# Performance work log

Measured on AMD Instinct MI355X. Metric: run time of the kernel, lower is better.

Reference implementation:

```python
import jax, jax.numpy as jnp
import numpy as np

VOCAB = 32
UTT_LEN = 16
NUM_MEANING_TYPES = 5
MEANINGS_PER_TYPE = 10
SUPPORT_SIZE = 100000  # = MEANINGS_PER_TYPE ** NUM_MEANING_TYPES
BATCH = 2048


def setup_inputs() -> dict:
    key = jax.random.key(0)
    k1, k2, k3 = jax.random.split(key, 3)
    # query utterances: [utt_len, batch] token ids
    utts = jax.random.randint(k1, (UTT_LEN, BATCH), 0, VOCAB, dtype=jnp.int64)
    # support set is stored as one-hot encoded utterances [S, utt_len*vocab]
    support_tokens = jax.random.randint(k2, (SUPPORT_SIZE, UTT_LEN), 0, VOCAB)
    support = jax.nn.one_hot(support_tokens, VOCAB, dtype=jnp.float32)
    support = support.reshape(SUPPORT_SIZE, UTT_LEN * VOCAB)
    # meanings table [S, num_meaning_types]
    meanings_t = jax.random.randint(k3, (SUPPORT_SIZE, NUM_MEANING_TYPES), 0,
                                    MEANINGS_PER_TYPE, dtype=jnp.int64)
    return {"utts": utts, "support": support, "meanings_t": meanings_t}


def reference(utts, support, meanings_t):
    # utts: [M, N] ints; support: [S, M*V] floats; meanings_t: [S, T] ints
    M, N = utts.shape
    # one-hot encode queries: [N, M, V] -> [N, M*V]
    batch_fluffy = jax.nn.one_hot(utts.T, VOCAB, dtype=jnp.float32).reshape(N, M * VOCAB)
    batch_sq = jnp.sum(batch_fluffy * batch_fluffy, axis=1)        # [N]
    support_sq = jnp.sum(support * support, axis=1)                # [S]
    cross = batch_fluffy @ support.T                                # [N, S]
    squared_dist = batch_sq[:, None] + support_sq[None, :] - 2.0 * cross
    # top-1 smallest distance (K=1)
    top1 = jnp.argmin(squared_dist, axis=1)                         # [N]
    meanings = meanings_t[top1]                                     # [N, T]
    return jax.nn.one_hot(meanings, MEANINGS_PER_TYPE, dtype=jnp.float32)
```

## Files before the change

### kernel.cpp

```cpp
#include <hip/hip_runtime.h>
#include <stdint.h>

#define S_ROWS 100000
#define NQ     2048
#define M_POS  16
#define VOCABS 32
#define WPB    8
#define GROUPS 8
#define CHUNKS 125
#define RC     800
#define KITER  25
#define KPAD   264

__global__ __launch_bounds__(256) void knn_decode(const float* __restrict__ support,
                                                  uint8_t* __restrict__ tok) {
    int wave = (blockIdx.x * 256 + threadIdx.x) >> 6;
    int lane = threadIdx.x & 63;
    if (wave >= S_ROWS) return;
    const float4* rowp = (const float4*)(support + (size_t)wave * 512) + lane * 2;
    float4 f0 = rowp[0];
    float4 f1 = rowp[1];
    float base = (float)((lane & 3) * 64);
    float v = f0.x * (base + 0.f)  + f0.y * (base + 8.f)  + f0.z * (base + 16.f) + f0.w * (base + 24.f)
            + f1.x * (base + 32.f) + f1.y * (base + 40.f) + f1.z * (base + 48.f) + f1.w * (base + 56.f);
    v += __shfl_xor(v, 1);
    v += __shfl_xor(v, 2);
    if ((lane & 3) == 0) {
        int p = lane >> 2;
        tok[(size_t)wave * 16 + p] = (uint8_t)(v + 0.5f);
    }
}

__device__ __forceinline__ void FA(uint32_t a, uint32_t b, uint32_t c,
                                   uint32_t& s, uint32_t& co) {
    uint32_t x = a ^ b;
    s  = x ^ c;
    co = (a & b) | (x & c);
}
__device__ __forceinline__ void HA(uint32_t a, uint32_t b, uint32_t& s, uint32_t& co) {
    s = a ^ b; co = a & b;
}

__global__ __launch_bounds__(256, 4) void knn_score(const int* __restrict__ utts,
                                                    const uint8_t* __restrict__ tok,
                                                    uint32_t* __restrict__ partial) {
    __shared__ uint32_t smem[32 * KPAD];
    uint32_t* table = smem;
    uint32_t* keys  = smem;

    const int bid = blockIdx.x;
    const int g   = bid & 7;
    const int c   = bid >> 3;
    const int t   = threadIdx.x;

    #pragma unroll
    for (int i = 0; i < 16; ++i) table[t + 256 * i] = 0u;
    __syncthreads();

    {
        int q = g * 256 + t;
        int wb = t >> 5, j = t & 31;
        #pragma unroll
        for (int m = 0; m < M_POS; ++m) {
            int v = utts[m * NQ + q];
            atomicOr(&table[(m * VOCABS + v) * WPB + wb], 1u << j);
        }
    }
    __syncthreads();

    const int w   = t & 7;
    const int sub = t >> 3;
    const int r0  = c * RC;
    const uint32_t* tw = table + w;

    uint32_t cp0=0,cp1=0,cp2=0,cp3=0,cp4=0;
    uint32_t k0p=0,k1p=0,k2p=0,k3p=0,k4p=0;

    const uint4* tbase = (const uint4*)(tok + (size_t)(r0 + sub) * 16);

    #pragma unroll
    for (int k = 0; k < KITER; ++k) {
        uint4 ta = tbase[32 * k];
        uint32_t b[16];
        b[0]  = tw[ (ta.x        & 0xFFu) +  0*256];
        b[1]  = tw[((ta.x >> 8)  & 0xFFu) +  1*256];
        b[2]  = tw[((ta.x >> 16) & 0xFFu) +  2*256];
        b[3]  = tw[((ta.x >> 24)        ) +  3*256];
        b[4]  = tw[ (ta.y        & 0xFFu) +  4*256];
        b[5]  = tw[((ta.y >> 8)  & 0xFFu) +  5*256];
        b[6]  = tw[((ta.y >> 16) & 0xFFu) +  6*256];
        b[7]  = tw[((ta.y >> 24)        ) +  7*256];
        b[8]  = tw[ (ta.z        & 0xFFu) +  8*256];
        b[9]  = tw[((ta.z >> 8)  & 0xFFu) +  9*256];
        b[10] = tw[((ta.z >> 16) & 0xFFu) + 10*256];
        b[11] = tw[((ta.z >> 24)        ) + 11*256];
        b[12] = tw[ (ta.w        & 0xFFu) + 12*256];
        b[13] = tw[((ta.w >> 8)  & 0xFFu) + 13*256];
        b[14] = tw[((ta.w >> 16) & 0xFFu) + 14*256];
        b[15] = tw[((ta.w >> 24)        ) + 15*256];

        uint32_t s10,s11,s12,s13,s14, c10,c11,c12,c13,c14;
        FA(b[0],b[1],b[2],   s10,c10);
        FA(b[3],b[4],b[5],   s11,c11);
        FA(b[6],b[7],b[8],   s12,c12);
        FA(b[9],b[10],b[11], s13,c13);
        FA(b[12],b[13],b[14],s14,c14);
        uint32_t s2a,c2a,s2b,c2b;
        FA(s10,s11,s12, s2a,c2a);
        FA(s13,s14,b[15], s2b,c2b);
        uint32_t n0,h0;  HA(s2a,s2b, n0,h0);
        uint32_t u,cu,vv,cv,x2,cx,n1,cy;
        FA(c10,c11,c12, u,cu);
        FA(c13,c14,c2a, vv,cv);
        FA(u,vv,c2b,    x2,cx);
        HA(x2,h0,       n1,cy);
        uint32_t y4,cz,n2,cw,n3,n4;
        FA(cu,cv,cx, y4,cz);
        HA(y4,cy,    n2,cw);
        HA(cz,cw,    n3,n4);

        uint32_t eq = ~(n4 ^ cp4);
        uint32_t gt = n4 & ~cp4;
        gt |= eq & (n3 & ~cp3);  eq &= ~(n3 ^ cp3);
        gt |= eq & (n2 & ~cp2);  eq &= ~(n2 ^ cp2);
        gt |= eq & (n1 & ~cp1);  eq &= ~(n1 ^ cp1);
        gt |= eq & (n0 & ~cp0);

        uint32_t ng = ~gt;
        cp0 = (gt & n0) | (ng & cp0);
        cp1 = (gt & n1) | (ng & cp1);
        cp2 = (gt & n2) | (ng & cp2);
        cp3 = (gt & n3) | (ng & cp3);
        cp4 = (gt & n4) | (ng & cp4);
        k0p = ( k       & 1) ? (k0p & ng) | gt : (k0p & ng);
        k1p = ((k >> 1) & 1) ? (k1p & ng) | gt : (k1p & ng);
        k2p = ((k >> 2) & 1) ? (k2p & ng) | gt : (k2p & ng);
        k3p = ((k >> 3) & 1) ? (k3p & ng) | gt : (k3p & ng);
        k4p = ((k >> 4) & 1) ? (k4p & ng) | gt : (k4p & ng);
    }

    __syncthreads();

    {
        uint32_t C = 0x1FFFFu - (uint32_t)(r0 + sub);
        #pragma unroll
        for (int j = 0; j < 32; ++j) {
            uint32_t cnt = ((cp0>>j)&1u) | (((cp1>>j)&1u)<<1) | (((cp2>>j)&1u)<<2)
                         | (((cp3>>j)&1u)<<3) | (((cp4>>j)&1u)<<4);
            uint32_t kk  = ((k0p>>j)&1u) | (((k1p>>j)&1u)<<1) | (((k2p>>j)&1u)<<2)
                         | (((k3p>>j)&1u)<<3) | (((k4p>>j)&1u)<<4);
            uint32_t key = (cnt << 17) + C - (kk << 5);
            keys[j * KPAD + t] = key;
        }
    }
    __syncthreads();

    {
        int w2 = t & 7, j2 = t >> 3;
        const uint32_t* kp = keys + j2 * KPAD + w2;
        uint32_t best = 0;
        #pragma unroll
        for (int i = 0; i < 32; ++i) {
            uint32_t v = kp[8 * i];
            best = best > v ? best : v;
        }
        partial[(size_t)c * NQ + g * 256 + w2 * 32 + j2] = best;
    }
}

__global__ __launch_bounds__(256) void knn_reduce_out(const uint32_t* __restrict__ partial,
                                                      const int* __restrict__ meanings,
                                                      float* __restrict__ out) {
    int q = blockIdx.x * 256 + threadIdx.x;
    if (q >= NQ) return;
    uint32_t best = 0;
    #pragma unroll 5
    for (int c = 0; c < CHUNKS; ++c) {
        uint32_t v = partial[(size_t)c * NQ + q];
        best = best > v ? best : v;
    }
    int idx = 0x1FFFF - (int)(best & 0x1FFFFu);
    float* o = out + (size_t)q * 50;
    #pragma unroll
    for (int tt = 0; tt < 5; ++tt) {
        int mv = meanings[(size_t)idx * 5 + tt];
        #pragma unroll
        for (int mm = 0; mm < 10; ++mm) o[tt * 10 + mm] = (mm == mv) ? 1.0f : 0.0f;
    }
}

extern "C" void kernel_launch(void* const* d_in, const int* in_sizes, int n_in,
                              void* d_out, int out_size, void* d_ws, size_t ws_size,
                              hipStream_t stream) {
    const int*   utts     = (const int*)d_in[0];
    const float* support  = (const float*)d_in[1];
    const int*   meanings = (const int*)d_in[2];
    float* out = (float*)d_out;

    uint8_t*  tok     = (uint8_t*)d_ws;
    uint32_t* partial = (uint32_t*)((char*)d_ws + (size_t)S_ROWS * 16);

    knn_decode<<<(S_ROWS + 3) / 4, 256, 0, stream>>>(support, tok);
    knn_score<<<GROUPS * CHUNKS, 256, 0, stream>>>(utts, tok, partial);
    knn_reduce_out<<<NQ / 256, 256, 0, stream>>>(partial, meanings, out);
}
```

Baseline: 324.9 us.

## Fuse support decode into scoring kernel with all queries per block

Drops the separate decode kernel and its token buffer: each 1024-thread block now decodes its support rows straight from the float one-hot data and scores them against bitsets for all 2048 queries, held in a 128KB shared-memory table. Each wave handles one row per pass, broadcasting decoded tokens with shuffles and looking up per-lane query words. This removes one launch and the tok write and read-back, and the grid shrinks to 250 blocks. The trade-offs are heavier shared-memory use per block, possible low occupancy, and the float loads now sit on the scoring critical path.

```diff
diff --git a/kernel.cpp b/kernel.cpp
--- a/kernel.cpp
+++ b/kernel.cpp
@@ -5,31 +5,9 @@
 #define NQ     2048
 #define M_POS  16
 #define VOCABS 32
-#define WPB    8
-#define GROUPS 8
-#define CHUNKS 125
-#define RC     800
-#define KITER  25
-#define KPAD   264
-
-__global__ __launch_bounds__(256) void knn_decode(const float* __restrict__ support,
-                                                  uint8_t* __restrict__ tok) {
-    int wave = (blockIdx.x * 256 + threadIdx.x) >> 6;
-    int lane = threadIdx.x & 63;
-    if (wave >= S_ROWS) return;
-    const float4* rowp = (const float4*)(support + (size_t)wave * 512) + lane * 2;
-    float4 f0 = rowp[0];
-    float4 f1 = rowp[1];
-    float base = (float)((lane & 3) * 64);
-    float v = f0.x * (base + 0.f)  + f0.y * (base + 8.f)  + f0.z * (base + 16.f) + f0.w * (base + 24.f)
-            + f1.x * (base + 32.f) + f1.y * (base + 40.f) + f1.z * (base + 48.f) + f1.w * (base + 56.f);
-    v += __shfl_xor(v, 1);
-    v += __shfl_xor(v, 2);
-    if ((lane & 3) == 0) {
-        int p = lane >> 2;
-        tok[(size_t)wave * 16 + p] = (uint8_t)(v + 0.5f);
-    }
-}
+#define BLOCKS 250
+#define RPB    400
+#define PASSES 25
 
 __device__ __forceinline__ void FA(uint32_t a, uint32_t b, uint32_t c,
                                    uint32_t& s, uint32_t& co) {
@@ -41,63 +19,57 @@
     s = a ^ b; co = a & b;
 }
 
-__global__ __launch_bounds__(256, 4) void knn_score(const int* __restrict__ utts,
-                                                    const uint8_t* __restrict__ tok,
-                                                    uint32_t* __restrict__ partial) {
-    __shared__ uint32_t smem[32 * KPAD];
-    uint32_t* table = smem;
-    uint32_t* keys  = smem;
+__global__ __launch_bounds__(1024, 4) void knn_fused(const int* __restrict__ utts,
+                                                     const float* __restrict__ support,
+                                                     uint32_t* __restrict__ partial) {
+    __shared__ uint32_t smem[32768];
 
-    const int bid = blockIdx.x;
-    const int g   = bid & 7;
-    const int c   = bid >> 3;
-    const int t   = threadIdx.x;
+    const int t = threadIdx.x;
+    const int c = blockIdx.x;
 
     #pragma unroll
-    for (int i = 0; i < 16; ++i) table[t + 256 * i] = 0u;
+    for (int i = 0; i < 8; ++i)
+        *(uint4*)&smem[t * 4 + i * 4096] = uint4{0u, 0u, 0u, 0u};
     __syncthreads();
 
-    {
-        int q = g * 256 + t;
-        int wb = t >> 5, j = t & 31;
+    #pragma unroll
+    for (int h = 0; h < 2; ++h) {
+        int q  = t + h * 1024;
+        int wd = q >> 5, bit = q & 31;
         #pragma unroll
         for (int m = 0; m < M_POS; ++m) {
             int v = utts[m * NQ + q];
-            atomicOr(&table[(m * VOCABS + v) * WPB + wb], 1u << j);
+            atomicOr(&smem[m * 2048 + v * 64 + wd], 1u << bit);
         }
     }
     __syncthreads();
 
-    const int w   = t & 7;
-    const int sub = t >> 3;
-    const int r0  = c * RC;
-    const uint32_t* tw = table + w;
+    const int wave = t >> 6;
+    const int lane = t & 63;
 
     uint32_t cp0=0,cp1=0,cp2=0,cp3=0,cp4=0;
     uint32_t k0p=0,k1p=0,k2p=0,k3p=0,k4p=0;
 
-    const uint4* tbase = (const uint4*)(tok + (size_t)(r0 + sub) * 16);
+    const float* rowbase = support + ((size_t)c * RPB + wave) * 512 + lane * 8;
 
     #pragma unroll
-    for (int k = 0; k < KITER; ++k) {
-        uint4 ta = tbase[32 * k];
+    for (int p = 0; p < PASSES; ++p) {
+        const float4* rp = (const float4*)(rowbase + (size_t)p * 16 * 512);
+        float4 f0 = rp[0];
+        float4 f1 = rp[1];
+        float base = (float)((lane & 3) * 64);
+        float v = f0.x * (base + 0.f)  + f0.y * (base + 8.f)  + f0.z * (base + 16.f) + f0.w * (base + 24.f)
+                + f1.x * (base + 32.f) + f1.y * (base + 40.f) + f1.z * (base + 48.f) + f1.w * (base + 56.f);
+        v += __shfl_xor(v, 1);
+        v += __shfl_xor(v, 2);
+        int tok8 = (int)(v + 0.5f);
+
         uint32_t b[16];
-        b[0]  = tw[ (ta.x        & 0xFFu) +  0*256];
-        b[1]  = tw[((ta.x >> 8)  & 0xFFu) +  1*256];
-        b[2]  = tw[((ta.x >> 16) & 0xFFu) +  2*256];
-        b[3]  = tw[((ta.x >> 24)        ) +  3*256];
-        b[4]  = tw[ (ta.y        & 0xFFu) +  4*256];
-        b[5]  = tw[((ta.y >> 8)  & 0xFFu) +  5*256];
-        b[6]  = tw[((ta.y >> 16) & 0xFFu) +  6*256];
-        b[7]  = tw[((ta.y >> 24)        ) +  7*256];
-        b[8]  = tw[ (ta.z        & 0xFFu) +  8*256];
-        b[9]  = tw[((ta.z >> 8)  & 0xFFu) +  9*256];
-        b[10] = tw[((ta.z >> 16) & 0xFFu) + 10*256];
-        b[11] = tw[((ta.z >> 24)        ) + 11*256];
-        b[12] = tw[ (ta.w        & 0xFFu) + 12*256];
-        b[13] = tw[((ta.w >> 8)  & 0xFFu) + 13*256];
-        b[14] = tw[((ta.w >> 16) & 0xFFu) + 14*256];
-        b[15] = tw[((ta.w >> 24)        ) + 15*256];
+        #pragma unroll
+        for (int m = 0; m < 16; ++m) {
+            uint32_t tm = (uint32_t)__shfl(tok8, 4 * m);
+            b[m] = smem[m * 2048 + tm * 8 + lane];
+        }
 
         uint32_t s10,s11,s12,s13,s14, c10,c11,c12,c13,c14;
         FA(b[0],b[1],b[2],   s10,c10);
@@ -132,39 +104,39 @@
         cp2 = (gt & n2) | (ng & cp2);
         cp3 = (gt & n3) | (ng & cp3);
         cp4 = (gt & n4) | (ng & cp4);
-        k0p = ( k       & 1) ? (k0p & ng) | gt : (k0p & ng);
-        k1p = ((k >> 1) & 1) ? (k1p & ng) | gt : (k1p & ng);
-        k2p = ((k >> 2) & 1) ? (k2p & ng) | gt : (k2p & ng);
-        k3p = ((k >> 3) & 1) ? (k3p & ng) | gt : (k3p & ng);
-        k4p = ((k >> 4) & 1) ? (k4p & ng) | gt : (k4p & ng);
+        k0p = ( p       & 1) ? (k0p & ng) | gt : (k0p & ng);
+        k1p = ((p >> 1) & 1) ? (k1p & ng) | gt : (k1p & ng);
+        k2p = ((p >> 2) & 1) ? (k2p & ng) | gt : (k2p & ng);
+        k3p = ((p >> 3) & 1) ? (k3p & ng) | gt : (k3p & ng);
+        k4p = ((p >> 4) & 1) ? (k4p & ng) | gt : (k4p & ng);
     }
 
     __syncthreads();
 
     {
-        uint32_t C = 0x1FFFFu - (uint32_t)(r0 + sub);
-        #pragma unroll
+        uint32_t C0 = 0x1FFFFu - (uint32_t)(c * RPB + wave);
+        #pragma unroll 1
         for (int j = 0; j < 32; ++j) {
             uint32_t cnt = ((cp0>>j)&1u) | (((cp1>>j)&1u)<<1) | (((cp2>>j)&1u)<<2)
                          | (((cp3>>j)&1u)<<3) | (((cp4>>j)&1u)<<4);
-            uint32_t kk  = ((k0p>>j)&1u) | (((k1p>>j)&1u)<<1) | (((k2p>>j)&1u)<<2)
+            uint32_t pw  = ((k0p>>j)&1u) | (((k1p>>j)&1u)<<1) | (((k2p>>j)&1u)<<2)
                          | (((k3p>>j)&1u)<<3) | (((k4p>>j)&1u)<<4);
-            uint32_t key = (cnt << 17) + C - (kk << 5);
-            keys[j * KPAD + t] = key;
+            smem[j * 1024 + t] = (cnt << 17) + C0 - (pw << 4);
         }
     }
     __syncthreads();
 
-    {
-        int w2 = t & 7, j2 = t >> 3;
-        const uint32_t* kp = keys + j2 * KPAD + w2;
+    #pragma unroll
+    for (int h = 0; h < 2; ++h) {
+        int j = (t >> 6) + h * 16;
+        int w = t & 63;
         uint32_t best = 0;
         #pragma unroll
-        for (int i = 0; i < 32; ++i) {
-            uint32_t v = kp[8 * i];
-            best = best > v ? best : v;
+        for (int v2 = 0; v2 < 16; ++v2) {
+            uint32_t x = smem[j * 1024 + v2 * 64 + w];
+            best = best > x ? best : x;
         }
-        partial[(size_t)c * NQ + g * 256 + w2 * 32 + j2] = best;
+        partial[(size_t)c * NQ + w * 32 + j] = best;
     }
 }
 
@@ -175,7 +147,7 @@
     if (q >= NQ) return;
     uint32_t best = 0;
     #pragma unroll 5
-    for (int c = 0; c < CHUNKS; ++c) {
+    for (int c = 0; c < BLOCKS; ++c) {
         uint32_t v = partial[(size_t)c * NQ + q];
         best = best > v ? best : v;
     }
@@ -197,10 +169,8 @@
     const int*   meanings = (const int*)d_in[2];
     float* out = (float*)d_out;
 
-    uint8_t*  tok     = (uint8_t*)d_ws;
-    uint32_t* partial = (uint32_t*)((char*)d_ws + (size_t)S_ROWS * 16);
+    uint32_t* partial = (uint32_t*)d_ws;
 
-    knn_decode<<<(S_ROWS + 3) / 4, 256, 0, stream>>>(support, tok);
-    knn_score<<<GROUPS * CHUNKS, 256, 0, stream>>>(utts, tok, partial);
+    knn_fused<<<BLOCKS, 1024, 0, stream>>>(utts, support, partial);
     knn_reduce_out<<<NQ / 256, 256, 0, stream>>>(partial, meanings, out);
 }
```

Measured after the change: 517.3 us. +59.2%, slower.
